# Kernel tuning notes

Measured on AMD Instinct MI355X. Metric: run time of the kernel, lower is better.

## Reference

```python
import jax, jax.numpy as jnp
import numpy as np

EPS = 1e-5

def _layernorm(h):
    # parameter-free LayerNorm over last dim (elementwise_affine=False)
    mu = jnp.mean(h, axis=-1, keepdims=True)
    var = jnp.mean(jnp.square(h - mu), axis=-1, keepdims=True)
    return (h - mu) / jnp.sqrt(var + EPS)

def setup_inputs() -> dict:
    key = jax.random.key(0)
    k1, k2, k3, k4 = jax.random.split(key, 4)
    B, D, F_, I = 16, 37, 4096, 64
    x = jax.random.normal(k1, (B, D, F_), dtype=jnp.float32)
    s = 1.0 / np.sqrt(D)  # ~ torch Linear default init scale
    Wq = jax.random.normal(k2, (D, I), dtype=jnp.float32) * s
    Wk = jax.random.normal(k3, (D, I), dtype=jnp.float32) * s
    Wv = jax.random.normal(k4, (D, I), dtype=jnp.float32) * s
    return {"x": x, "Wq": Wq, "Wk": Wk, "Wv": Wv}

def reference(x, Wq, Wk, Wv):
    # x: [B, depth, featuresize] -> entities [B, F, depth]
    xb = jnp.transpose(x, (0, 2, 1))
    q = _layernorm(jnp.einsum('bfd,di->bfi', xb, Wq))
    k = _layernorm(jnp.einsum('bfd,di->bfi', xb, Wk))
    v = _layernorm(jnp.einsum('bfd,di->bfi', xb, Wv))
    d = q.shape[-1]
    att = jnp.einsum('bqi,bki->bqk', q, k) / jnp.sqrt(jnp.float32(d))
    # faithful to torch: softmax over dim=1 (the query axis), not the key axis
    weights = jax.nn.softmax(att, axis=-2)
    return jnp.einsum('bqk,bki->bqi', weights, v)
```

## Files before the change

kernel.cpp:

```cpp
#include <hip/hip_runtime.h>
#include <math.h>

#define B_  16
#define D_  37
#define F_  4096
#define I_  64
#define EPS 1e-5f
#define QSCALE 0.18033688011112042f
#define NQS 2

typedef unsigned short u16;
typedef __bf16 bf16x8 __attribute__((ext_vector_type(8)));
typedef float  f32x16 __attribute__((ext_vector_type(16)));
typedef unsigned int u32x4 __attribute__((ext_vector_type(4)));
typedef int i32x2 __attribute__((ext_vector_type(2)));

#define ZERO16 {0,0,0,0, 0,0,0,0, 0,0,0,0, 0,0,0,0}
#define MFMA32(a, b, c) __builtin_amdgcn_mfma_f32_32x32x16_bf16((a), (b), (c), 0, 0, 0)

#if __has_builtin(__builtin_amdgcn_exp2f)
#define EX2(x) __builtin_amdgcn_exp2f(x)
#else
#define EX2(x) exp2f(x)
#endif
#if __has_builtin(__builtin_amdgcn_rcpf)
#define RCP(x) __builtin_amdgcn_rcpf(x)
#else
#define RCP(x) (1.f / (x))
#endif

__device__ __forceinline__ u16 f2b(float f) {
  unsigned u = __builtin_bit_cast(unsigned, f);
  return (u16)((u + 0x7fffu + ((u >> 16) & 1u)) >> 16);
}
__device__ __forceinline__ unsigned pk2(float lo, float hi) {
  unsigned a = __builtin_bit_cast(unsigned, lo);
  unsigned b = __builtin_bit_cast(unsigned, hi);
  return ((b + 0x8000u) & 0xffff0000u) | ((a + 0x8000u) >> 16);
}

__device__ __forceinline__ void plswap(unsigned& a, unsigned& b) {
#if __has_builtin(__builtin_amdgcn_permlane32_swap)
  i32x2 r = __builtin_amdgcn_permlane32_swap((int)a, (int)b, false, false);
  a = (unsigned)r[0];
  b = (unsigned)r[1];
#else
  const int lh = (int)((threadIdx.x & 63) >> 5);
  unsigned pa = (unsigned)__shfl_xor((int)a, 32, 64);
  unsigned pb = (unsigned)__shfl_xor((int)b, 32, 64);
  unsigned na = lh ? pb : a;
  unsigned nb = lh ? b : pa;
  a = na;
  b = nb;
#endif
}

__device__ __forceinline__ void build_af(const f32x16& s, bf16x8& f0, bf16x8& f1) {
  float e[16];
#pragma unroll
  for (int r = 0; r < 16; ++r) e[r] = EX2(s[r]);
  unsigned a = pk2(e[0], e[1]),   bq = pk2(e[2], e[3]);
  unsigned c = pk2(e[4], e[5]),   d  = pk2(e[6], e[7]);
  plswap(a, c);
  plswap(bq, d);
  u32x4 v0 = {a, bq, c, d};
  f0 = __builtin_bit_cast(bf16x8, v0);
  unsigned ee = pk2(e[8], e[9]),  ff = pk2(e[10], e[11]);
  unsigned g  = pk2(e[12], e[13]), h = pk2(e[14], e[15]);
  plswap(ee, g);
  plswap(ff, h);
  u32x4 v1 = {ee, ff, g, h};
  f1 = __builtin_bit_cast(bf16x8, v1);
}

__device__ __forceinline__ bf16x8 ldfrag(const u16* base, int row, int kb) {
  return *(const bf16x8*)(base + (row << 6) + ((kb ^ (row & 7)) << 3));
}
__device__ __forceinline__ void stage16(u16* dst, const u16* src, int c, int spitch) {
  const int r = c >> 3, cb = c & 7;
  const int4 v = *(const int4*)(src + (size_t)r * spitch + (cb << 3));
  *(int4*)(dst + (r << 6) + ((cb ^ (r & 7)) << 3)) = v;
}

__global__ __launch_bounds__(256) void qkv_ln_k(
    const float* __restrict__ x,
    const float* __restrict__ Wq, const float* __restrict__ Wk,
    const float* __restrict__ Wv,
    u16* __restrict__ qn, u16* __restrict__ kn, u16* __restrict__ vt) {
  __shared__ float sW[3 * D_ * I_];
  __shared__ float xs[D_ * 64];
  __shared__ __align__(16) u16 vtile[64 * 72];

  const int t = threadIdx.x;
  const int b = blockIdx.y;
  const int f0 = blockIdx.x * 64;

  for (int i = t; i < D_ * I_; i += 256) {
    sW[i]               = Wq[i];
    sW[D_ * I_ + i]     = Wk[i];
    sW[2 * D_ * I_ + i] = Wv[i];
  }
  const float* xb = x + (size_t)b * D_ * F_ + f0;
  for (int i = t; i < D_ * 64; i += 256)
    xs[i] = xb[(size_t)(i >> 6) * F_ + (i & 63)];
  __syncthreads();

  const int lane = t & 63, w = t >> 6;

  for (int it = 0; it < 16; ++it) {
    const int fl = w * 16 + it;
    float hq = 0.f, hk = 0.f, hv = 0.f;
#pragma unroll
    for (int d = 0; d < D_; ++d) {
      const float xv = xs[d * 64 + fl];
      hq = fmaf(xv, sW[d * 64 + lane], hq);
      hk = fmaf(xv, sW[D_ * I_ + d * 64 + lane], hk);
      hv = fmaf(xv, sW[2 * D_ * I_ + d * 64 + lane], hv);
    }
    auto lnorm = [&](float a) -> float {
      float s = a;
#pragma unroll
      for (int o = 32; o > 0; o >>= 1) s += __shfl_xor(s, o, 64);
      const float mu = s * (1.f / 64.f);
      const float d0 = a - mu;
      float v = d0 * d0;
#pragma unroll
      for (int o = 32; o > 0; o >>= 1) v += __shfl_xor(v, o, 64);
      return d0 * rsqrtf(v * (1.f / 64.f) + EPS);
    };
    const size_t fo = ((size_t)b * F_ + f0 + fl) * I_ + lane;
    qn[fo] = f2b(lnorm(hq) * QSCALE);
    kn[fo] = f2b(lnorm(hk));
    vtile[lane * 72 + fl] = f2b(lnorm(hv));
  }
  __syncthreads();
  for (int p = 0; p < 2; ++p) {
    const int c = p * 256 + t;
    const int r = c >> 3, off = (c & 7) * 8;
    const int4 v = *(const int4*)&vtile[r * 72 + off];
    *(int4*)(vt + ((size_t)b * I_ + r) * F_ + f0 + off) = v;
  }
}

__global__ __launch_bounds__(512, 4) void attn_stats_k(
    const u16* __restrict__ qn, const u16* __restrict__ kn,
    float* __restrict__ zp) {
  __shared__ __align__(16) u16 sm[16384];

  const int t = threadIdx.x, lane = t & 63, w = t >> 6;
  const int l31 = lane & 31, lh = lane >> 5;
  const int b = blockIdx.y, k0 = blockIdx.x * 256, qh = blockIdx.z;

  const u16* kb = kn + ((size_t)b * F_ + k0) * I_;
#pragma unroll
  for (int p = 0; p < 4; ++p) stage16(sm, kb, p * 512 + t, 64);
  __syncthreads();
  const u16* myK = sm + (w * 32) * 64;
  bf16x8 kf[4];
#pragma unroll
  for (int ic = 0; ic < 4; ++ic) kf[ic] = ldfrag(myK, l31, ic * 2 + lh);
  __syncthreads();

  const u16* qb = qn + ((size_t)b * F_ + qh * (F_ / NQS)) * I_;
  stage16(sm, qb, t, 64);

  float Zc[4] = {0.f, 0.f, 0.f, 0.f};
  const int NC = F_ / NQS / 64;

  for (int c = 0; c < NC; ++c) {
    const u16* cur = sm + (c & 1) * 4096;
    u16* nxt = sm + ((c & 1) ^ 1) * 4096;
    __syncthreads();
    if (c + 1 < NC) stage16(nxt, qb + (size_t)(c + 1) * 64 * I_, t, 64);

    f32x16 a0 = ZERO16, a1 = ZERO16;
#pragma unroll
    for (int ic = 0; ic < 4; ++ic) {
      const bf16x8 q0f = ldfrag(cur, l31, ic * 2 + lh);
      const bf16x8 q1f = ldfrag(cur + 32 * 64, l31, ic * 2 + lh);
      a0 = MFMA32(q0f, kf[ic], a0);
      a1 = MFMA32(q1f, kf[ic], a1);
    }
#pragma unroll
    for (int r = 0; r < 16; ++r) {
      Zc[r & 3] += EX2(a0[r]);
      Zc[r & 3] += EX2(a1[r]);
    }
  }

  float Zt = (Zc[0] + Zc[1]) + (Zc[2] + Zc[3]);
  Zt += __shfl_xor(Zt, 32, 64);
  if (lane < 32)
    zp[((size_t)qh * B_ + b) * F_ + k0 + w * 32 + lane] = Zt;
}

__global__ __launch_bounds__(256) void vscale_k(u16* __restrict__ vt,
                                                const float* __restrict__ zp) {
  const int b = blockIdx.y;
  const int off = (blockIdx.x * 256 + (int)threadIdx.x) * 8;
  const int k = off & (F_ - 1);
  u16* p = vt + (size_t)b * I_ * F_ + off;
  const float* z0 = zp + (size_t)b * F_ + k;
  const float* z1 = zp + (size_t)B_ * F_ + (size_t)b * F_ + k;
  int4 raw = *(const int4*)p;
  u16 es[8], os[8];
  *(int4*)es = raw;
#pragma unroll
  for (int j = 0; j < 8; ++j) {
    const float v = __builtin_bit_cast(float, (unsigned)es[j] << 16);
    const float rz = RCP(z0[j] + z1[j]);
    os[j] = f2b(v * rz);
  }
  *(int4*)p = *(int4*)os;
}

__global__ __launch_bounds__(256, 3) void attn_out_k(
    const u16* __restrict__ qn, const u16* __restrict__ kn,
    const u16* __restrict__ vt, float* __restrict__ outp,
    float* __restrict__ pout) {
  __shared__ __align__(16) u16 sm[16384];

  const int t = threadIdx.x, lane = t & 63, w = t >> 6;
  const int l31 = lane & 31, lh = lane >> 5;
  const int b = blockIdx.y, q0 = blockIdx.x * 128, ks = blockIdx.z;

  const u16* qb = qn + ((size_t)b * F_ + q0) * I_;
#pragma unroll
  for (int p = 0; p < 4; ++p) stage16(sm, qb, p * 256 + t, 64);
  __syncthreads();
  const u16* myQ = sm + (w * 32) * 64;
  bf16x8 qf[4];
#pragma unroll
  for (int ic = 0; ic < 4; ++ic) qf[ic] = ldfrag(myQ, l31, ic * 2 + lh);
  __syncthreads();

  const u16* kbase = kn + ((size_t)b * F_ + ks * (F_ / 2)) * I_;
  const u16* vbase = vt + (size_t)b * I_ * F_ + ks * (F_ / 2);

#pragma unroll
  for (int p = 0; p < 2; ++p) {
    stage16(sm, kbase, p * 256 + t, 64);
    stage16(sm + 8192, vbase, p * 256 + t, F_);
  }

  f32x16 o0 = ZERO16, o1 = ZERO16;
  const int NCH = F_ / 2 / 64;

  for (int c = 0; c < NCH; ++c) {
    const int cur = (c & 1) * 4096;
    const int nxt = cur ^ 4096;
    __syncthreads();
    if (c + 1 < NCH) {
#pragma unroll
      for (int p = 0; p < 2; ++p) {
        stage16(sm + nxt, kbase + (size_t)(c + 1) * 64 * I_, p * 256 + t, 64);
        stage16(sm + 8192 + nxt, vbase + (size_t)(c + 1) * 64, p * 256 + t, F_);
      }
    }

    const u16* Kc = sm + cur;
    f32x16 s0 = ZERO16, s1 = ZERO16;
#pragma unroll
    for (int ic = 0; ic < 4; ++ic) {
      const bf16x8 ak0 = ldfrag(Kc, l31, ic * 2 + lh);
      const bf16x8 ak1 = ldfrag(Kc + 32 * 64, l31, ic * 2 + lh);
      s0 = MFMA32(ak0, qf[ic], s0);
      s1 = MFMA32(ak1, qf[ic], s1);
    }

    bf16x8 af[4];
    build_af(s0, af[0], af[1]);
    build_af(s1, af[2], af[3]);

    const u16* Vc = sm + 8192 + cur;
#pragma unroll
    for (int kb4 = 0; kb4 < 4; ++kb4) {
      const bf16x8 bv0 = ldfrag(Vc, l31, kb4 * 2 + lh);
      const bf16x8 bv1 = ldfrag(Vc + 32 * 64, l31, kb4 * 2 + lh);
      o0 = MFMA32(af[kb4], bv0, o0);
      o1 = MFMA32(af[kb4], bv1, o1);
    }
  }

  float* dst = (ks == 0 ? outp : pout) + ((size_t)b * F_ + q0 + w * 32) * I_;
#pragma unroll
  for (int r = 0; r < 16; ++r) {
    const int qr = (r & 3) + 8 * (r >> 2) + 4 * lh;
    dst[(size_t)qr * I_ + l31]      = o0[r];
    dst[(size_t)qr * I_ + 32 + l31] = o1[r];
  }
}

__global__ __launch_bounds__(256) void reduce_k(float* __restrict__ outp,
                                                const float* __restrict__ p1) {
  const size_t i = ((size_t)blockIdx.x * 256 + threadIdx.x) * 4;
  float4 a = *(const float4*)(outp + i);
  const float4 bq = *(const float4*)(p1 + i);
  a.x += bq.x; a.y += bq.y; a.z += bq.z; a.w += bq.w;
  *(float4*)(outp + i) = a;
}

extern "C" void kernel_launch(void* const* d_in, const int* in_sizes, int n_in,
                              void* d_out, int out_size, void* d_ws,
                              size_t ws_size, hipStream_t stream) {
  const float* x  = (const float*)d_in[0];
  const float* Wq = (const float*)d_in[1];
  const float* Wk = (const float*)d_in[2];
  const float* Wv = (const float*)d_in[3];
  float* out = (float*)d_out;

  const size_t NBF = (size_t)B_ * F_ * I_;
  u16* qn    = (u16*)d_ws;
  u16* kn    = qn + NBF;
  u16* vt    = kn + NBF;
  float* zp  = (float*)(vt + NBF);
  float* pout = zp + (size_t)NQS * B_ * F_;

  qkv_ln_k<<<dim3(F_ / 64, B_), 256, 0, stream>>>(x, Wq, Wk, Wv, qn, kn, vt);
  attn_stats_k<<<dim3(F_ / 256, B_, NQS), 512, 0, stream>>>(qn, kn, zp);
  vscale_k<<<dim3(I_ * F_ / 2048, B_), 256, 0, stream>>>(vt, zp);
  attn_out_k<<<dim3(F_ / 128, B_, 2), 256, 0, stream>>>(qn, kn, vt, out, pout);
  reduce_k<<<dim3((int)(NBF / 1024)), 256, 0, stream>>>(out, pout);
}
```

Before: 258.0 us.

## Give each wave two 32-row tiles in attention kernels and drop split-K reduce

Both attention kernels now have each wave own 64 rows (two 32-row MFMA tiles) instead of 32. Staged Q/K/V fragments are reused across twice as many MFMAs, and the kernels run with half as many threads per block. The attention-output kernel no longer splits the key range in two, which removes the partial-output buffer and the separate reduce kernel. The bf16 packing now uses a hardware conversion, and load offsets are precomputed once. In exchange there is more register pressure, fewer waves in flight, and only 512 output blocks, which may reduce occupancy and latency hiding.

```diff
diff --git a/kernel.cpp b/kernel.cpp
--- a/kernel.cpp
+++ b/kernel.cpp
@@ -11,7 +11,9 @@
 
 typedef unsigned short u16;
 typedef __bf16 bf16x8 __attribute__((ext_vector_type(8)));
+typedef __bf16 bf16x2v __attribute__((ext_vector_type(2)));
 typedef float  f32x16 __attribute__((ext_vector_type(16)));
+typedef float  f32x2v __attribute__((ext_vector_type(2)));
 typedef unsigned int u32x4 __attribute__((ext_vector_type(4)));
 typedef int i32x2 __attribute__((ext_vector_type(2)));
 
@@ -34,9 +36,9 @@
   return (u16)((u + 0x7fffu + ((u >> 16) & 1u)) >> 16);
 }
 __device__ __forceinline__ unsigned pk2(float lo, float hi) {
-  unsigned a = __builtin_bit_cast(unsigned, lo);
-  unsigned b = __builtin_bit_cast(unsigned, hi);
-  return ((b + 0x8000u) & 0xffff0000u) | ((a + 0x8000u) >> 16);
+  f32x2v f = {lo, hi};
+  bf16x2v h = __builtin_convertvector(f, bf16x2v);
+  return __builtin_bit_cast(unsigned, h);
 }
 
 __device__ __forceinline__ void plswap(unsigned& a, unsigned& b) {
@@ -81,6 +83,13 @@
   const int4 v = *(const int4*)(src + (size_t)r * spitch + (cb << 3));
   *(int4*)(dst + (r << 6) + ((cb ^ (r & 7)) << 3)) = v;
 }
+__device__ __forceinline__ int soff_l(int c) {
+  const int r = c >> 3, cb = c & 7;
+  return (r << 6) + ((cb ^ (r & 7)) << 3);
+}
+__device__ __forceinline__ int soff_g(int c, int spitch) {
+  return (c >> 3) * spitch + ((c & 7) << 3);
+}
 
 __global__ __launch_bounds__(256) void qkv_ln_k(
     const float* __restrict__ x,
@@ -142,7 +151,7 @@
   }
 }
 
-__global__ __launch_bounds__(512, 4) void attn_stats_k(
+__global__ __launch_bounds__(256, 2) void attn_stats_k(
     const u16* __restrict__ qn, const u16* __restrict__ kn,
     float* __restrict__ zp) {
   __shared__ __align__(16) u16 sm[16384];
@@ -153,45 +162,70 @@
 
   const u16* kb = kn + ((size_t)b * F_ + k0) * I_;
 #pragma unroll
-  for (int p = 0; p < 4; ++p) stage16(sm, kb, p * 512 + t, 64);
-  __syncthreads();
-  const u16* myK = sm + (w * 32) * 64;
-  bf16x8 kf[4];
-#pragma unroll
-  for (int ic = 0; ic < 4; ++ic) kf[ic] = ldfrag(myK, l31, ic * 2 + lh);
-  __syncthreads();
-
-  const u16* qb = qn + ((size_t)b * F_ + qh * (F_ / NQS)) * I_;
-  stage16(sm, qb, t, 64);
-
-  float Zc[4] = {0.f, 0.f, 0.f, 0.f};
+  for (int p = 0; p < 8; ++p) stage16(sm, kb, p * 256 + t, 64);
+  __syncthreads();
+  bf16x8 kf[2][4];
+#pragma unroll
+  for (int kb2 = 0; kb2 < 2; ++kb2)
+#pragma unroll
+    for (int ic = 0; ic < 4; ++ic)
+      kf[kb2][ic] = ldfrag(sm + (w * 64 + kb2 * 32) * 64, l31, ic * 2 + lh);
+  __syncthreads();
+
+  int qoff_l[2], qoff_g[2];
+#pragma unroll
+  for (int p = 0; p < 2; ++p) {
+    const int c = p * 256 + t;
+    qoff_l[p] = soff_l(c);
+    qoff_g[p] = soff_g(c, 64);
+  }
+
+  const u16* qsrc = qn + ((size_t)b * F_ + qh * (F_ / NQS)) * I_;
+#pragma unroll
+  for (int p = 0; p < 2; ++p)
+    *(int4*)(sm + qoff_l[p]) = *(const int4*)(qsrc + qoff_g[p]);
+  qsrc += 64 * I_;
+
+  float Zc[2][2] = {{0.f, 0.f}, {0.f, 0.f}};
   const int NC = F_ / NQS / 64;
 
   for (int c = 0; c < NC; ++c) {
-    const u16* cur = sm + (c & 1) * 4096;
-    u16* nxt = sm + ((c & 1) ^ 1) * 4096;
+    const int cur = (c & 1) * 4096;
     __syncthreads();
-    if (c + 1 < NC) stage16(nxt, qb + (size_t)(c + 1) * 64 * I_, t, 64);
-
-    f32x16 a0 = ZERO16, a1 = ZERO16;
+    if (c + 1 < NC) {
+      const int nxt = cur ^ 4096;
+#pragma unroll
+      for (int p = 0; p < 2; ++p)
+        *(int4*)(sm + nxt + qoff_l[p]) = *(const int4*)(qsrc + qoff_g[p]);
+      qsrc += 64 * I_;
+    }
+
+    f32x16 a00 = ZERO16, a01 = ZERO16, a10 = ZERO16, a11 = ZERO16;
 #pragma unroll
     for (int ic = 0; ic < 4; ++ic) {
-      const bf16x8 q0f = ldfrag(cur, l31, ic * 2 + lh);
-      const bf16x8 q1f = ldfrag(cur + 32 * 64, l31, ic * 2 + lh);
-      a0 = MFMA32(q0f, kf[ic], a0);
-      a1 = MFMA32(q1f, kf[ic], a1);
+      const bf16x8 q0f = ldfrag(sm + cur, l31, ic * 2 + lh);
+      const bf16x8 q1f = ldfrag(sm + cur + 32 * 64, l31, ic * 2 + lh);
+      a00 = MFMA32(q0f, kf[0][ic], a00);
+      a01 = MFMA32(q0f, kf[1][ic], a01);
+      a10 = MFMA32(q1f, kf[0][ic], a10);
+      a11 = MFMA32(q1f, kf[1][ic], a11);
     }
 #pragma unroll
     for (int r = 0; r < 16; ++r) {
-      Zc[r & 3] += EX2(a0[r]);
-      Zc[r & 3] += EX2(a1[r]);
-    }
-  }
-
-  float Zt = (Zc[0] + Zc[1]) + (Zc[2] + Zc[3]);
-  Zt += __shfl_xor(Zt, 32, 64);
-  if (lane < 32)
-    zp[((size_t)qh * B_ + b) * F_ + k0 + w * 32 + lane] = Zt;
+      Zc[0][0] += EX2(a00[r]);
+      Zc[0][1] += EX2(a01[r]);
+      Zc[1][0] += EX2(a10[r]);
+      Zc[1][1] += EX2(a11[r]);
+    }
+  }
+
+#pragma unroll
+  for (int kb2 = 0; kb2 < 2; ++kb2) {
+    float Zt = Zc[0][kb2] + Zc[1][kb2];
+    Zt += __shfl_xor(Zt, 32, 64);
+    if (lane < 32)
+      zp[((size_t)qh * B_ + b) * F_ + k0 + w * 64 + kb2 * 32 + lane] = Zt;
+  }
 }
 
 __global__ __launch_bounds__(256) void vscale_k(u16* __restrict__ vt,
@@ -214,90 +248,102 @@
   *(int4*)p = *(int4*)os;
 }
 
-__global__ __launch_bounds__(256, 3) void attn_out_k(
+__global__ __launch_bounds__(128, 2) void attn_out_k(
     const u16* __restrict__ qn, const u16* __restrict__ kn,
-    const u16* __restrict__ vt, float* __restrict__ outp,
-    float* __restrict__ pout) {
+    const u16* __restrict__ vt, float* __restrict__ out) {
   __shared__ __align__(16) u16 sm[16384];
 
   const int t = threadIdx.x, lane = t & 63, w = t >> 6;
   const int l31 = lane & 31, lh = lane >> 5;
-  const int b = blockIdx.y, q0 = blockIdx.x * 128, ks = blockIdx.z;
+  const int b = blockIdx.y, q0 = blockIdx.x * 128;
 
   const u16* qb = qn + ((size_t)b * F_ + q0) * I_;
 #pragma unroll
-  for (int p = 0; p < 4; ++p) stage16(sm, qb, p * 256 + t, 64);
-  __syncthreads();
-  const u16* myQ = sm + (w * 32) * 64;
-  bf16x8 qf[4];
-#pragma unroll
-  for (int ic = 0; ic < 4; ++ic) qf[ic] = ldfrag(myQ, l31, ic * 2 + lh);
-  __syncthreads();
-
-  const u16* kbase = kn + ((size_t)b * F_ + ks * (F_ / 2)) * I_;
-  const u16* vbase = vt + (size_t)b * I_ * F_ + ks * (F_ / 2);
-
-#pragma unroll
-  for (int p = 0; p < 2; ++p) {
-    stage16(sm, kbase, p * 256 + t, 64);
-    stage16(sm + 8192, vbase, p * 256 + t, F_);
-  }
-
-  f32x16 o0 = ZERO16, o1 = ZERO16;
-  const int NCH = F_ / 2 / 64;
-
-  for (int c = 0; c < NCH; ++c) {
+  for (int p = 0; p < 8; ++p) stage16(sm, qb, p * 128 + t, 64);
+  __syncthreads();
+  bf16x8 qf[2][4];
+#pragma unroll
+  for (int qb2 = 0; qb2 < 2; ++qb2)
+#pragma unroll
+    for (int ic = 0; ic < 4; ++ic)
+      qf[qb2][ic] = ldfrag(sm + (w * 64 + qb2 * 32) * 64, l31, ic * 2 + lh);
+  __syncthreads();
+
+  int off_l[4], kg[4], vg[4];
+#pragma unroll
+  for (int p = 0; p < 4; ++p) {
+    const int c = p * 128 + t;
+    off_l[p] = soff_l(c);
+    kg[p] = soff_g(c, 64);
+    vg[p] = soff_g(c, F_);
+  }
+
+  const u16* ksrc = kn + (size_t)b * F_ * I_;
+  const u16* vsrc = vt + (size_t)b * I_ * F_;
+#pragma unroll
+  for (int p = 0; p < 4; ++p) {
+    *(int4*)(sm + off_l[p])        = *(const int4*)(ksrc + kg[p]);
+    *(int4*)(sm + 8192 + off_l[p]) = *(const int4*)(vsrc + vg[p]);
+  }
+  ksrc += 64 * I_;
+  vsrc += 64;
+
+  f32x16 o00 = ZERO16, o01 = ZERO16, o10 = ZERO16, o11 = ZERO16;
+  const int NC = F_ / 64;
+
+  for (int c = 0; c < NC; ++c) {
     const int cur = (c & 1) * 4096;
-    const int nxt = cur ^ 4096;
     __syncthreads();
-    if (c + 1 < NCH) {
-#pragma unroll
-      for (int p = 0; p < 2; ++p) {
-        stage16(sm + nxt, kbase + (size_t)(c + 1) * 64 * I_, p * 256 + t, 64);
-        stage16(sm + 8192 + nxt, vbase + (size_t)(c + 1) * 64, p * 256 + t, F_);
+    if (c + 1 < NC) {
+      const int nxt = cur ^ 4096;
+#pragma unroll
+      for (int p = 0; p < 4; ++p) {
+        *(int4*)(sm + nxt + off_l[p])        = *(const int4*)(ksrc + kg[p]);
+        *(int4*)(sm + 8192 + nxt + off_l[p]) = *(const int4*)(vsrc + vg[p]);
       }
+      ksrc += 64 * I_;
+      vsrc += 64;
     }
 
     const u16* Kc = sm + cur;
-    f32x16 s0 = ZERO16, s1 = ZERO16;
+    f32x16 s00 = ZERO16, s01 = ZERO16, s10 = ZERO16, s11 = ZERO16;
 #pragma unroll
     for (int ic = 0; ic < 4; ++ic) {
       const bf16x8 ak0 = ldfrag(Kc, l31, ic * 2 + lh);
       const bf16x8 ak1 = ldfrag(Kc + 32 * 64, l31, ic * 2 + lh);
-      s0 = MFMA32(ak0, qf[ic], s0);
-      s1 = MFMA32(ak1, qf[ic], s1);
-    }
-
-    bf16x8 af[4];
-    build_af(s0, af[0], af[1]);
-    build_af(s1, af[2], af[3]);
+      s00 = MFMA32(ak0, qf[0][ic], s00);
+      s01 = MFMA32(ak0, qf[1][ic], s01);
+      s10 = MFMA32(ak1, qf[0][ic], s10);
+      s11 = MFMA32(ak1, qf[1][ic], s11);
+    }
+
+    bf16x8 af[2][4];
+    build_af(s00, af[0][0], af[0][1]);
+    build_af(s10, af[0][2], af[0][3]);
+    build_af(s01, af[1][0], af[1][1]);
+    build_af(s11, af[1][2], af[1][3]);
 
     const u16* Vc = sm + 8192 + cur;
 #pragma unroll
     for (int kb4 = 0; kb4 < 4; ++kb4) {
       const bf16x8 bv0 = ldfrag(Vc, l31, kb4 * 2 + lh);
       const bf16x8 bv1 = ldfrag(Vc + 32 * 64, l31, kb4 * 2 + lh);
-      o0 = MFMA32(af[kb4], bv0, o0);
-      o1 = MFMA32(af[kb4], bv1, o1);
-    }
-  }
-
-  float* dst = (ks == 0 ? outp : pout) + ((size_t)b * F_ + q0 + w * 32) * I_;
+      o00 = MFMA32(af[0][kb4], bv0, o00);
+      o01 = MFMA32(af[0][kb4], bv1, o01);
+      o10 = MFMA32(af[1][kb4], bv0, o10);
+      o11 = MFMA32(af[1][kb4], bv1, o11);
+    }
+  }
+
+  float* ob = out + ((size_t)b * F_ + q0 + w * 64) * I_;
 #pragma unroll
   for (int r = 0; r < 16; ++r) {
     const int qr = (r & 3) + 8 * (r >> 2) + 4 * lh;
-    dst[(size_t)qr * I_ + l31]      = o0[r];
-    dst[(size_t)qr * I_ + 32 + l31] = o1[r];
-  }
-}
-
-__global__ __launch_bounds__(256) void reduce_k(float* __restrict__ outp,
-                                                const float* __restrict__ p1) {
-  const size_t i = ((size_t)blockIdx.x * 256 + threadIdx.x) * 4;
-  float4 a = *(const float4*)(outp + i);
-  const float4 bq = *(const float4*)(p1 + i);
-  a.x += bq.x; a.y += bq.y; a.z += bq.z; a.w += bq.w;
-  *(float4*)(outp + i) = a;
+    ob[(size_t)qr * I_ + l31]              = o00[r];
+    ob[(size_t)qr * I_ + 32 + l31]         = o01[r];
+    ob[(size_t)(32 + qr) * I_ + l31]       = o10[r];
+    ob[(size_t)(32 + qr) * I_ + 32 + l31]  = o11[r];
+  }
 }
 
 extern "C" void kernel_launch(void* const* d_in, const int* in_sizes, int n_in,
@@ -310,15 +356,13 @@
   float* out = (float*)d_out;
 
   const size_t NBF = (size_t)B_ * F_ * I_;
-  u16* qn    = (u16*)d_ws;
-  u16* kn    = qn + NBF;
-  u16* vt    = kn + NBF;
-  float* zp  = (float*)(vt + NBF);
-  float* pout = zp + (size_t)NQS * B_ * F_;
+  u16* qn   = (u16*)d_ws;
+  u16* kn   = qn + NBF;
+  u16* vt   = kn + NBF;
+  float* zp = (float*)(vt + NBF);
 
   qkv_ln_k<<<dim3(F_ / 64, B_), 256, 0, stream>>>(x, Wq, Wk, Wv, qn, kn, vt);
-  attn_stats_k<<<dim3(F_ / 256, B_, NQS), 512, 0, stream>>>(qn, kn, zp);
+  attn_stats_k<<<dim3(F_ / 256, B_, NQS), 256, 0, stream>>>(qn, kn, zp);
   vscale_k<<<dim3(I_ * F_ / 2048, B_), 256, 0, stream>>>(vt, zp);
-  attn_out_k<<<dim3(F_ / 128, B_, 2), 256, 0, stream>>>(qn, kn, vt, out, pout);
-  reduce_k<<<dim3((int)(NBF / 1024)), 256, 0, stream>>>(out, pout);
-}
+  attn_out_k<<<dim3(F_ / 128, B_), 128, 0, stream>>>(qn, kn, vt, out);
+}
```

Result: slower. 273.5 us (+6.0%).
